# Performance work log

Hardware: AMD Instinct MI355X
Metric: run time of the kernel (lower is better)

Reference implementation:

```python
import math
import jax, jax.numpy as jnp
import numpy as np

PE_DIM = 128
NUM_HEADS = 8
U = V = 2
TEMP = 10000.0


def sine_pe(y_embed, x_embed, num_pos_feats, temperature, card):
    """Matches get_sine_position_encoding with use_norm=True."""
    eps = 1e-6
    scale = 2.0 * math.pi
    y = y_embed / (card[0] + eps) * scale
    x = x_embed / (card[1] + eps) * scale
    dim_t = jnp.asarray(temperature, jnp.float32) ** (
        2.0 * (jnp.arange(num_pos_feats, dtype=jnp.float32) // 2) / num_pos_feats)
    px = x[..., None] / dim_t
    py = y[..., None] / dim_t

    def interleave(p):
        s = jnp.sin(p[..., 0::2])
        c = jnp.cos(p[..., 1::2])
        return jnp.stack((s, c), axis=-1).reshape(p.shape[:-1] + (-1,))

    return jnp.concatenate((interleave(py), interleave(px)), axis=-1)


def setup_inputs() -> dict:
    key = jax.random.key(0)
    ks = jax.random.split(key, 8)
    B, C, H, W = 2, 64, 256, 256
    dim = C
    # xavier-ish scale for Linear(128 -> 64)
    w_std = math.sqrt(2.0 / (PE_DIM + dim))
    return {
        "feat_supp": jax.random.normal(ks[0], (B, C, H, W), jnp.float32),
        "flow": jax.random.normal(ks[1], (B, H, W, 2), jnp.float32) * 3.0,
        "feat_curr": jax.random.normal(ks[2], (B, C, H, W), jnp.float32),
        "q_w": jax.random.normal(ks[3], (dim, PE_DIM), jnp.float32) * w_std,
        "q_b": jnp.zeros((dim,), jnp.float32),
        "k_w": jax.random.normal(ks[4], (dim, PE_DIM), jnp.float32) * w_std,
        "k_b": jnp.zeros((dim,), jnp.float32),
        "v_w": jax.random.normal(ks[5], (dim, PE_DIM), jnp.float32) * w_std,
        "v_b": jnp.zeros((dim,), jnp.float32),
    }


def reference(feat_supp, flow, feat_curr, q_w, q_b, k_w, k_b, v_w, v_b):
    B, C, H, W = feat_curr.shape
    UV = U * V
    HW = H * W
    nh = NUM_HEADS
    hd = C // nh
    d = PE_DIM // C  # pe channels per feature channel
    scale = hd ** (-0.5)

    # flow-displaced integer grid + fractional part
    img_off = jnp.stack(
        jnp.meshgrid(jnp.arange(H), jnp.arange(W), indexing="ij"), axis=-1
    ).astype(flow.dtype)                                   # (H, W, 2) in (y, x)
    grid_full = img_off[None] + flow[..., ::-1]            # flow flipped to (y, x)
    grid_intg = jnp.floor(grid_full).astype(jnp.int32)
    grid_deci = grid_full - grid_intg                      # (B, H, W, 2)

    win_off = jnp.stack(
        jnp.meshgrid(jnp.arange(U), jnp.arange(V), indexing="ij"), axis=-1
    ).astype(jnp.int32)                                    # (U, V, 2)
    grid_w = grid_intg[:, :, :, None, None, :] + win_off[None, None, None]
    grid_w = grid_w.reshape(B, HW * UV, 2)
    deci = grid_deci.reshape(B, HW, 2)

    # duplicate-padding gather of support features
    h_idx = jnp.clip(grid_w[..., 0], 0, H - 1)
    w_idx = jnp.clip(grid_w[..., 1], 0, W - 1)
    lin = h_idx * W + w_idx                                # (B, HW*UV)
    feat_warp = jnp.take_along_axis(
        feat_supp.reshape(B, C, HW), lin[:, None, :], axis=2)  # (B, C, HW*UV)
    feat_warp = feat_warp.transpose(0, 2, 1).reshape(B, HW, UV, C)

    # window position bias (card = window_size - 1, use_corrected_card=False)
    wy, wx = jnp.meshgrid(jnp.arange(U, dtype=jnp.float32),
                          jnp.arange(V, dtype=jnp.float32), indexing="ij")
    pos_bias = sine_pe(wy.reshape(1, -1), wx.reshape(1, -1),
                       PE_DIM // 2, TEMP, (U - 1, V - 1))   # (1, UV, PE_DIM)
    pe_warp = pos_bias.reshape(1, 1, UV, C, d)
    fw = (feat_warp[..., None] + pe_warp).reshape(B, HW, UV, PE_DIM)

    # current-frame features + fractional-offset positional encoding
    fc = feat_curr.reshape(B, C, HW).transpose(0, 2, 1)     # (B, HW, C)
    pe_curr = sine_pe(deci[..., 0], deci[..., 1],
                      PE_DIM // 2, TEMP, (U, V))            # (B, HW, PE_DIM)
    fc = (fc[..., None] + pe_curr.reshape(B, HW, C, d)).reshape(B, HW, PE_DIM)

    q = (fc @ q_w.T + q_b).reshape(B, HW, nh, hd)
    k = (fw @ k_w.T + k_b).reshape(B, HW, UV, nh, hd)
    v = (fw @ v_w.T + v_b).reshape(B, HW, UV, nh, hd)

    attn = jnp.einsum("bnhd,bnuhd->bnhu", q * scale, k)
    attn = jax.nn.softmax(attn, axis=-1)
    out = jnp.einsum("bnhu,bnuhd->bnhd", attn, v).reshape(B, HW, C)
    return out.reshape(B, H, W, C).transpose(0, 3, 1, 2)
```

## Files before the change

### kernel.cpp

```cpp
#include <hip/hip_runtime.h>
#include <hip/hip_bf16.h>

#define HWHW 65536
#define LN1E4_32 0.28782313662425572f
#define TWO_PI_N 6.2831847f

typedef __attribute__((ext_vector_type(8))) short short8;
typedef __attribute__((ext_vector_type(4))) short s16x4;
typedef __attribute__((ext_vector_type(4))) float f32x4;


__device__ __forceinline__ short f2bf(float f) {
  union { __hip_bfloat16 h; short s; } u;
  u.h = __float2bfloat16(f);
  return u.s;
}

__global__ __launch_bounds__(256)
void pre_pass(const float* __restrict__ supp,
              const float* __restrict__ qw, const float* __restrict__ kw,
              const float* __restrict__ vw,
              const float* __restrict__ kb, const float* __restrict__ vb,
              __hip_bfloat16* __restrict__ suppT,
              __hip_bfloat16* __restrict__ wfrag, float* __restrict__ bias) {
  const int t = threadIdx.x;
  if (blockIdx.x < 2048) {
    __shared__ short tile[64 * 68];
    const int b   = blockIdx.x >> 10;
    const int p0  = (blockIdx.x & 1023) << 6;
    const int px4 = (t & 15) << 2;
    const int g   = t >> 4;

    const float* src = supp + ((size_t)b * 64 + g * 4) * HWHW + p0 + px4;
    f32x4 v[4];
#pragma unroll
    for (int c = 0; c < 4; ++c)
      v[c] = *(const f32x4*)(src + (size_t)c * HWHW);
#pragma unroll
    for (int j = 0; j < 4; ++j) {
      s16x4 pk;
#pragma unroll
      for (int c = 0; c < 4; ++c) pk[c] = f2bf(v[c][j]);
      *(s16x4*)&tile[(px4 + j) * 68 + g * 4] = pk;
    }
    __syncthreads();
    const int px = t >> 2, ch0 = (t & 3) << 4;
    s16x4 r0 = *(s16x4*)&tile[px * 68 + ch0];
    s16x4 r1 = *(s16x4*)&tile[px * 68 + ch0 + 4];
    s16x4 r2 = *(s16x4*)&tile[px * 68 + ch0 + 8];
    s16x4 r3 = *(s16x4*)&tile[px * 68 + ch0 + 12];
    short8 o0, o1;
#pragma unroll
    for (int j = 0; j < 4; ++j) {
      o0[j] = r0[j]; o0[j + 4] = r1[j];
      o1[j] = r2[j]; o1[j + 4] = r3[j];
    }
    short8* dst = (short8*)(suppT + ((size_t)(b * HWHW + p0 + px)) * 64 + ch0);
    dst[0] = o0;
    dst[1] = o1;
  } else if (blockIdx.x < 2056) {
    int slot = (blockIdx.x - 2048) * 256 + t;
    __hip_bfloat16* dst = wfrag + slot * 8;
    if (slot < 1024) {
      int ksnt = slot >> 6, lane = slot & 63;
      int ks = ksnt >> 2, nt = ksnt & 3;
      const float* w = qw + (nt * 16 + (lane & 15)) * 128 + ks * 32 + (lane >> 4) * 8;
#pragma unroll
      for (int j = 0; j < 8; ++j) dst[j] = __float2bfloat16(w[j]);
    } else {
      int mat = (slot >= 1536);
      int rem = slot & 511;
      int ksnt = rem >> 6, lane = rem & 63;
      int ks = ksnt >> 2, nt = ksnt & 3;
      int c0 = ks * 32 + (lane >> 4) * 8;
      const float* w = (mat ? vw : kw) + (nt * 16 + (lane & 15)) * 128;
#pragma unroll
      for (int j = 0; j < 8; ++j)
        dst[j] = __float2bfloat16(w[2 * (c0 + j)] + w[2 * (c0 + j) + 1]);
    }
  } else {
    for (int s = t; s < 512; s += 256) {
      int mat = s >> 8, uv = (s >> 6) & 3, c = s & 63;
      const float* w = (mat ? vw : kw) + c * 128;
      float acc = (mat ? vb : kb)[c];
      for (int kk = 0; kk < 128; ++kk) {
        float val = (kk < 64 ? (float)(uv >> 1) : (float)(uv & 1)) * TWO_PI_N;
        int i = kk & 63, f = i >> 1;
        float arg = val * __expf(-(float)f * LN1E4_32);
        float pe = (i & 1) ? __cosf(arg) : __sinf(arg);
        acc += pe * w[kk];
      }
      bias[s] = acc;
    }
  }
}

__global__ __attribute__((amdgpu_waves_per_eu(5, 8))) __launch_bounds__(256)
void iw_main(const __hip_bfloat16* __restrict__ suppT, const float* __restrict__ flow,
             const float* __restrict__ feat_curr,
             const short8* __restrict__ wg, const float* __restrict__ bias_g,
             const float* __restrict__ q_b, float* __restrict__ out)
{
  __shared__ __align__(16) char smem[18688];
  f32x4* lds_bias = (f32x4*)smem;
  float* outstage = (float*)(smem + 2048);

  const int tid = threadIdx.x;
  const int idx = ((blockIdx.x & 7) << 8) | (blockIdx.x >> 3);
  const int b   = idx >> 10;
  const int hw0 = (idx & 1023) << 6;
  const int lane = tid & 63, wv = tid >> 6;
  const int quad = lane >> 4, l15 = lane & 15;
  const int uvl  = l15 & 3;
  const int prow = l15 >> 2;
  const short8* sT = (const short8*)suppT;

  {
    float* bl = (float*)lds_bias;
#pragma unroll
    for (int s_ = 0; s_ < 2; ++s_) {
      int s = s_ * 256 + tid;
      int mat = s >> 8, rem = s & 255, r = rem >> 6, c = rem & 63;
      bl[mat * 256 + (c >> 4) * 64 + (c & 15) * 4 + r] = bias_g[s];
    }
  }
  __syncthreads();

  float invd[2][4];
#pragma unroll
  for (int a = 0; a < 2; ++a)
#pragma unroll
    for (int jj = 0; jj < 4; ++jj)
      invd[a][jj] = __expf(-(float)(a * 16 + quad * 4 + jj) * LN1E4_32);

  int iy, ix;
  f32x4 qacc[4];

  {
    const int qpix = hw0 + wv * 16 + l15;
    float2 fl = ((const float2*)flow)[b * HWHW + qpix];
    float gy = (float)(qpix >> 8) + fl.y;
    float gx = (float)(qpix & 255) + fl.x;
    float fy = floorf(gy), fx = floorf(gx);
    iy = (int)fy; ix = (int)fx;
    float vy = (gy - fy) * (6.2831853071795864f / 2.000001f);
    float vx = (gx - fx) * (6.2831853071795864f / 2.000001f);

    short8 qa[4];
#pragma unroll
    for (int ks = 0; ks < 4; ++ks) {
      float val = (ks < 2) ? vy : vx;
#pragma unroll
      for (int jj = 0; jj < 4; ++jj) {
        int c = ks * 16 + quad * 4 + jj;
        float feat = feat_curr[(b * 64 + c) * HWHW + qpix];
        float arg = val * invd[ks & 1][jj];
        qa[ks][jj * 2]     = f2bf(feat + __sinf(arg));
        qa[ks][jj * 2 + 1] = f2bf(feat + __cosf(arg));
      }
    }
#pragma unroll
    for (int nt = 0; nt < 4; ++nt) qacc[nt] = (f32x4){0.f, 0.f, 0.f, 0.f};

    short8 qw0[4], qw1[4];
#pragma unroll
    for (int i = 0; i < 4; ++i) qw0[i] = wg[i * 64 + lane];
#pragma unroll
    for (int ks = 0; ks < 4; ++ks) {
      if (ks < 3) {
        short8* dstw = (ks & 1) ? qw0 : qw1;
#pragma unroll
        for (int i = 0; i < 4; ++i) dstw[i] = wg[((ks + 1) * 4 + i) * 64 + lane];
      }
      const short8* qw = (ks & 1) ? qw1 : qw0;
#pragma unroll
      for (int nt = 0; nt < 4; ++nt)
        qacc[nt] = __builtin_amdgcn_mfma_f32_16x16x32_bf16(
            qa[ks], qw[nt], qacc[nt], 0, 0, 0);
    }
  }

  int off[4];
#pragma unroll
  for (int m = 0; m < 4; ++m) {
    int p  = m * 4 + prow;
    int yy = min(max(__shfl(iy, p) + (uvl >> 1), 0), 255);
    int xx = min(max(__shfl(ix, p) + (uvl & 1), 0), 255);
    off[m] = (b * HWHW + yy * 256 + xx) * 8;
  }

  short8 ka[4][2];
#pragma unroll
  for (int m = 0; m < 4; ++m) {
    ka[m][0] = sT[off[m] + quad];
    ka[m][1] = sT[off[m] + 4 + quad];
  }

  float qT[4][4];
  {
#pragma unroll
    for (int nt = 0; nt < 4; ++nt) {
      float qb = q_b[nt * 16 + l15];
#pragma unroll
      for (int r = 0; r < 4; ++r)
        qacc[nt][r] = (qacc[nt][r] + qb) * 0.35355339059327373f;
    }
#pragma unroll
    for (int mt = 0; mt < 4; ++mt)
#pragma unroll
      for (int nt = 0; nt < 4; ++nt) {
        int src = mt * 16 + l15;
        float v0 = __shfl(qacc[nt][0], src);
        float v1 = __shfl(qacc[nt][1], src);
        float v2 = __shfl(qacc[nt][2], src);
        float v3 = __shfl(qacc[nt][3], src);
        float t0 = (quad & 2) ? v2 : v0;
        float t1 = (quad & 2) ? v3 : v1;
        qT[mt][nt] = (quad & 1) ? t1 : t0;
      }
  }

#pragma unroll
  for (int nt = 0; nt < 4; ++nt) {
    short8 kf0 = wg[1024 + nt * 64 + lane];
    short8 kf1 = wg[1024 + (4 + nt) * 64 + lane];
    short8 vf0 = wg[1024 + (8 + nt) * 64 + lane];
    short8 vf1 = wg[1024 + (12 + nt) * 64 + lane];
    f32x4 kb4 = lds_bias[nt * 16 + l15];
    f32x4 vb4 = lds_bias[64 + nt * 16 + l15];

#pragma unroll
    for (int mt = 0; mt < 4; ++mt) {
      f32x4 kacc = kb4;
      f32x4 vacc = vb4;
      kacc = __builtin_amdgcn_mfma_f32_16x16x32_bf16(ka[mt][0], kf0, kacc, 0, 0, 0);
      kacc = __builtin_amdgcn_mfma_f32_16x16x32_bf16(ka[mt][1], kf1, kacc, 0, 0, 0);
      vacc = __builtin_amdgcn_mfma_f32_16x16x32_bf16(ka[mt][0], vf0, vacc, 0, 0, 0);
      vacc = __builtin_amdgcn_mfma_f32_16x16x32_bf16(ka[mt][1], vf1, vacc, 0, 0, 0);

      float lg[4];
#pragma unroll
      for (int r = 0; r < 4; ++r) {
        float p = qT[mt][nt] * kacc[r];
        p += __int_as_float(__builtin_amdgcn_update_dpp(
                 0, __float_as_int(p), 0xB1, 0xf, 0xf, true));
        p += __int_as_float(__builtin_amdgcn_update_dpp(
                 0, __float_as_int(p), 0x4E, 0xf, 0xf, true));
        p += __int_as_float(__builtin_amdgcn_update_dpp(
                 0, __float_as_int(p), 0x141, 0xf, 0xf, true));
        lg[r] = p;
      }
      float mx = fmaxf(fmaxf(lg[0], lg[1]), fmaxf(lg[2], lg[3]));
      float e0 = __expf(lg[0] - mx), e1 = __expf(lg[1] - mx);
      float e2 = __expf(lg[2] - mx), e3 = __expf(lg[3] - mx);
      float inv = 1.0f / (e0 + e1 + e2 + e3);
      float o = (e0 * vacc[0] + e1 * vacc[1] + e2 * vacc[2] + e3 * vacc[3]) * inv;
      outstage[(nt * 16 + l15) * 65 + wv * 16 + mt * 4 + quad] = o;
    }
  }

  __syncthreads();
#pragma unroll
  for (int i = 0; i < 16; ++i) {
    int j = i * 256 + tid;
    int c = j >> 6, p = j & 63;
    out[(b * 64 + c) * HWHW + hw0 + p] = outstage[c * 65 + p];
  }
}

extern "C" void kernel_launch(void* const* d_in, const int* in_sizes, int n_in,
                              void* d_out, int out_size, void* d_ws, size_t ws_size,
                              hipStream_t stream) {
  const float* feat_supp = (const float*)d_in[0];
  const float* flow      = (const float*)d_in[1];
  const float* feat_curr = (const float*)d_in[2];
  const float* q_w = (const float*)d_in[3];
  const float* q_b = (const float*)d_in[4];
  const float* k_w = (const float*)d_in[5];
  const float* k_b = (const float*)d_in[6];
  const float* v_w = (const float*)d_in[7];
  const float* v_b = (const float*)d_in[8];
  float* out = (float*)d_out;
  (void)in_sizes; (void)n_in; (void)out_size; (void)ws_size;

  __hip_bfloat16* wfrag = (__hip_bfloat16*)d_ws;
  float* bias           = (float*)((char*)d_ws + 32768);
  __hip_bfloat16* suppT = (__hip_bfloat16*)((char*)d_ws + 65536);

  hipLaunchKernelGGL(pre_pass, dim3(2057), dim3(256), 0, stream,
                     feat_supp, q_w, k_w, v_w, k_b, v_b, suppT, wfrag, bias);
  hipLaunchKernelGGL(iw_main, dim3(2048), dim3(256), 0, stream,
                     suppT, flow, feat_curr, (const short8*)d_ws, bias, q_b, out);
}
```

Measured before the change: 159.2 us.

## Stage projection weights in LDS and split output staging into two halves

Each block now copies the Q weight fragments into LDS and then the K/V fragments into the same buffer, so the MFMA B-operands come from LDS instead of per-wave global loads. The output staging buffer is halved: channels are processed in two 32-channel halves with a skewed (rotated) index in place of the +1 padding, each half written out before the next. This adds several __syncthreads barriers and grows LDS use to about 26KB, which may lower occupancy.

```diff
diff --git a/kernel.cpp b/kernel.cpp
--- a/kernel.cpp
+++ b/kernel.cpp
@@ -101,9 +101,10 @@
              const short8* __restrict__ wg, const float* __restrict__ bias_g,
              const float* __restrict__ q_b, float* __restrict__ out)
 {
-  __shared__ __align__(16) char smem[18688];
-  f32x4* lds_bias = (f32x4*)smem;
-  float* outstage = (float*)(smem + 2048);
+  __shared__ __align__(16) char smem[26624];
+  short8* lds_w    = (short8*)smem;
+  f32x4*  lds_bias = (f32x4*)(smem + 16384);
+  float*  outst    = (float*)(smem + 18432);
 
   const int tid = threadIdx.x;
   const int idx = ((blockIdx.x & 7) << 8) | (blockIdx.x >> 3);
@@ -115,6 +116,9 @@
   const int prow = l15 >> 2;
   const short8* sT = (const short8*)suppT;
 
+#pragma unroll
+  for (int j = 0; j < 4; ++j)
+    lds_w[j * 256 + tid] = wg[j * 256 + tid];
   {
     float* bl = (float*)lds_bias;
 #pragma unroll
@@ -161,23 +165,12 @@
     }
 #pragma unroll
     for (int nt = 0; nt < 4; ++nt) qacc[nt] = (f32x4){0.f, 0.f, 0.f, 0.f};
-
-    short8 qw0[4], qw1[4];
-#pragma unroll
-    for (int i = 0; i < 4; ++i) qw0[i] = wg[i * 64 + lane];
-#pragma unroll
-    for (int ks = 0; ks < 4; ++ks) {
-      if (ks < 3) {
-        short8* dstw = (ks & 1) ? qw0 : qw1;
-#pragma unroll
-        for (int i = 0; i < 4; ++i) dstw[i] = wg[((ks + 1) * 4 + i) * 64 + lane];
-      }
-      const short8* qw = (ks & 1) ? qw1 : qw0;
+#pragma unroll
+    for (int ks = 0; ks < 4; ++ks)
 #pragma unroll
       for (int nt = 0; nt < 4; ++nt)
         qacc[nt] = __builtin_amdgcn_mfma_f32_16x16x32_bf16(
-            qa[ks], qw[nt], qacc[nt], 0, 0, 0);
-    }
+            qa[ks], lds_w[(ks * 4 + nt) * 64 + lane], qacc[nt], 0, 0, 0);
   }
 
   int off[4];
@@ -189,6 +182,12 @@
     off[m] = (b * HWHW + yy * 256 + xx) * 8;
   }
 
+  __syncthreads();
+
+  short8 s0 = wg[1024 + tid];
+  short8 s1 = wg[1280 + tid];
+  short8 s2 = wg[1536 + tid];
+  short8 s3 = wg[1792 + tid];
   short8 ka[4][2];
 #pragma unroll
   for (int m = 0; m < 4; ++m) {
@@ -220,51 +219,63 @@
       }
   }
 
-#pragma unroll
-  for (int nt = 0; nt < 4; ++nt) {
-    short8 kf0 = wg[1024 + nt * 64 + lane];
-    short8 kf1 = wg[1024 + (4 + nt) * 64 + lane];
-    short8 vf0 = wg[1024 + (8 + nt) * 64 + lane];
-    short8 vf1 = wg[1024 + (12 + nt) * 64 + lane];
-    f32x4 kb4 = lds_bias[nt * 16 + l15];
-    f32x4 vb4 = lds_bias[64 + nt * 16 + l15];
-
-#pragma unroll
-    for (int mt = 0; mt < 4; ++mt) {
-      f32x4 kacc = kb4;
-      f32x4 vacc = vb4;
-      kacc = __builtin_amdgcn_mfma_f32_16x16x32_bf16(ka[mt][0], kf0, kacc, 0, 0, 0);
-      kacc = __builtin_amdgcn_mfma_f32_16x16x32_bf16(ka[mt][1], kf1, kacc, 0, 0, 0);
-      vacc = __builtin_amdgcn_mfma_f32_16x16x32_bf16(ka[mt][0], vf0, vacc, 0, 0, 0);
-      vacc = __builtin_amdgcn_mfma_f32_16x16x32_bf16(ka[mt][1], vf1, vacc, 0, 0, 0);
-
-      float lg[4];
-#pragma unroll
-      for (int r = 0; r < 4; ++r) {
-        float p = qT[mt][nt] * kacc[r];
-        p += __int_as_float(__builtin_amdgcn_update_dpp(
-                 0, __float_as_int(p), 0xB1, 0xf, 0xf, true));
-        p += __int_as_float(__builtin_amdgcn_update_dpp(
-                 0, __float_as_int(p), 0x4E, 0xf, 0xf, true));
-        p += __int_as_float(__builtin_amdgcn_update_dpp(
-                 0, __float_as_int(p), 0x141, 0xf, 0xf, true));
-        lg[r] = p;
+  lds_w[tid]       = s0;
+  lds_w[256 + tid] = s1;
+  lds_w[512 + tid] = s2;
+  lds_w[768 + tid] = s3;
+  __syncthreads();
+
+#pragma unroll
+  for (int half = 0; half < 2; ++half) {
+#pragma unroll
+    for (int nth = 0; nth < 2; ++nth) {
+      const int nt = half * 2 + nth;
+      short8 kf0 = lds_w[nt * 64 + lane];
+      short8 kf1 = lds_w[(4 + nt) * 64 + lane];
+      short8 vf0 = lds_w[(8 + nt) * 64 + lane];
+      short8 vf1 = lds_w[(12 + nt) * 64 + lane];
+      f32x4 kb4 = lds_bias[nt * 16 + l15];
+      f32x4 vb4 = lds_bias[64 + nt * 16 + l15];
+
+#pragma unroll
+      for (int mt = 0; mt < 4; ++mt) {
+        f32x4 kacc = kb4;
+        f32x4 vacc = vb4;
+        kacc = __builtin_amdgcn_mfma_f32_16x16x32_bf16(ka[mt][0], kf0, kacc, 0, 0, 0);
+        kacc = __builtin_amdgcn_mfma_f32_16x16x32_bf16(ka[mt][1], kf1, kacc, 0, 0, 0);
+        vacc = __builtin_amdgcn_mfma_f32_16x16x32_bf16(ka[mt][0], vf0, vacc, 0, 0, 0);
+        vacc = __builtin_amdgcn_mfma_f32_16x16x32_bf16(ka[mt][1], vf1, vacc, 0, 0, 0);
+
+        float lg[4];
+#pragma unroll
+        for (int r = 0; r < 4; ++r) {
+          float p = qT[mt][nt] * kacc[r];
+          p += __int_as_float(__builtin_amdgcn_update_dpp(
+                   0, __float_as_int(p), 0xB1, 0xf, 0xf, true));
+          p += __int_as_float(__builtin_amdgcn_update_dpp(
+                   0, __float_as_int(p), 0x4E, 0xf, 0xf, true));
+          p += __int_as_float(__builtin_amdgcn_update_dpp(
+                   0, __float_as_int(p), 0x141, 0xf, 0xf, true));
+          lg[r] = p;
+        }
+        float mx = fmaxf(fmaxf(lg[0], lg[1]), fmaxf(lg[2], lg[3]));
+        float e0 = __expf(lg[0] - mx), e1 = __expf(lg[1] - mx);
+        float e2 = __expf(lg[2] - mx), e3 = __expf(lg[3] - mx);
+        float inv = 1.0f / (e0 + e1 + e2 + e3);
+        float o = (e0 * vacc[0] + e1 * vacc[1] + e2 * vacc[2] + e3 * vacc[3]) * inv;
+        int c = nt * 16 + l15;
+        int p_ = wv * 16 + mt * 4 + quad;
+        outst[((nt & 1) * 16 + l15) * 64 + ((p_ + c) & 63)] = o;
       }
-      float mx = fmaxf(fmaxf(lg[0], lg[1]), fmaxf(lg[2], lg[3]));
-      float e0 = __expf(lg[0] - mx), e1 = __expf(lg[1] - mx);
-      float e2 = __expf(lg[2] - mx), e3 = __expf(lg[3] - mx);
-      float inv = 1.0f / (e0 + e1 + e2 + e3);
-      float o = (e0 * vacc[0] + e1 * vacc[1] + e2 * vacc[2] + e3 * vacc[3]) * inv;
-      outstage[(nt * 16 + l15) * 65 + wv * 16 + mt * 4 + quad] = o;
-    }
-  }
-
-  __syncthreads();
-#pragma unroll
-  for (int i = 0; i < 16; ++i) {
-    int j = i * 256 + tid;
-    int c = j >> 6, p = j & 63;
-    out[(b * 64 + c) * HWHW + hw0 + p] = outstage[c * 65 + p];
+    }
+    __syncthreads();
+#pragma unroll
+    for (int i = 0; i < 8; ++i) {
+      int r = i * 4 + wv;
+      int c = half * 32 + r;
+      out[(b * 64 + c) * HWHW + hw0 + lane] = outst[r * 64 + ((lane + c) & 63)];
+    }
+    if (half == 0) __syncthreads();
   }
 }
 
```

After: 163.9 us. +2.9%, slower.
